# Performance work log

Hardware: AMD Instinct MI355X
Metric: run time of the kernel (lower is better)

Reference implementation:

```python
import jax, jax.numpy as jnp
import numpy as np

FEAT_STRIDE = 16
PRE_NMS = 6000
POST_NMS = 300
NMS_THRESH = 0.7


def _whctrs(a):
    w = a[2] - a[0] + 1.0
    h = a[3] - a[1] + 1.0
    return w, h, a[0] + 0.5 * (w - 1), a[1] + 0.5 * (h - 1)

def _mkanchors(ws, hs, xc, yc):
    return np.stack([xc - 0.5 * (ws - 1), yc - 0.5 * (hs - 1),
                     xc + 0.5 * (ws - 1), yc + 0.5 * (hs - 1)], axis=1)

def _ratio_enum(anchor, ratios):
    w, h, xc, yc = _whctrs(anchor)
    size = w * h
    ws = np.round(np.sqrt(size / ratios))
    hs = np.round(ws * ratios)
    return _mkanchors(ws, hs, xc, yc)

def _scale_enum(anchor, scales):
    w, h, xc, yc = _whctrs(anchor)
    return _mkanchors(w * scales, h * scales, xc, yc)

def generate_anchors(base_size=16, ratios=np.array([0.5, 1.0, 2.0]), scales=np.array([8, 16, 32])):
    base = np.array([1, 1, base_size, base_size], dtype=np.float64) - 1
    ra = _ratio_enum(base, np.asarray(ratios, np.float64))
    return np.vstack([_scale_enum(ra[i], np.asarray(scales, np.float64)) for i in range(ra.shape[0])])


def setup_inputs() -> dict:
    key = jax.random.key(0)
    k1, k2 = jax.random.split(key)
    B, A, H, W = 8, 9, 64, 64
    scores = jax.random.normal(k1, (B, 2 * A, H, W), jnp.float32)
    bbox_deltas = jax.random.normal(k2, (B, 4 * A, H, W), jnp.float32)
    anchors = jnp.asarray(generate_anchors(16), jnp.float32)  # [9, 4]
    return {"scores": scores, "bbox_deltas": bbox_deltas, "anchors": anchors,
            "image_width": 1024, "image_height": 1024}


def _nms_keep(iou, thresh):
    # greedy NMS on score-sorted boxes given a full IoU matrix
    n = iou.shape[0]
    idx = jnp.arange(n)
    def body(i, keep):
        sup = keep[i] & (iou[i] > thresh) & (idx > i)
        return keep & ~sup
    return jax.lax.fori_loop(0, n, body, jnp.ones((n,), bool))


def _nms_one(boxes):  # boxes [PRE_NMS, 4], sorted by score desc
    b = jax.lax.stop_gradient(boxes)
    area = (b[:, 2] - b[:, 0] + 1.0) * (b[:, 3] - b[:, 1] + 1.0)
    iw = jnp.clip(jnp.minimum(b[:, None, 2], b[None, :, 2]) -
                  jnp.maximum(b[:, None, 0], b[None, :, 0]) + 1.0, 0.0)
    ih = jnp.clip(jnp.minimum(b[:, None, 3], b[None, :, 3]) -
                  jnp.maximum(b[:, None, 1], b[None, :, 1]) + 1.0, 0.0)
    inter = iw * ih
    iou = inter / (area[:, None] + area[None, :] - inter)
    keep = _nms_keep(iou, NMS_THRESH)
    # compact kept boxes to the front, pad with zeros (fixed shape)
    rank = jnp.cumsum(keep) - 1
    dest = jnp.where(keep, rank, PRE_NMS)  # suppressed -> dump row
    out = jnp.zeros((PRE_NMS + 1, 4), boxes.dtype).at[dest].set(boxes)
    return out[:POST_NMS]


def _forward(scores, bbox_deltas, anchors, image_width, image_height):
    B = scores.shape[0]
    A = anchors.shape[0]
    H, W = scores.shape[2], scores.shape[3]
    fg = scores[:, A:, :, :]                                   # [B, A, H, W]
    # shifted anchor grid
    mx, my = jnp.meshgrid(jnp.arange(W) * FEAT_STRIDE, jnp.arange(H) * FEAT_STRIDE)
    shifts = jnp.stack([mx.ravel(), my.ravel(), mx.ravel(), my.ravel()], 1).astype(scores.dtype)
    all_anchors = (shifts[:, None, :] + anchors[None, :, :]).reshape(-1, 4)  # [K*A, 4]
    deltas = bbox_deltas.transpose(0, 2, 3, 1).reshape(B, -1, 4)             # [B, K*A, 4]
    sc = fg.transpose(0, 2, 3, 1).reshape(B, -1)                             # [B, K*A]
    # bbox_transform_inv
    aw = all_anchors[:, 2] - all_anchors[:, 0] + 1.0
    ah = all_anchors[:, 3] - all_anchors[:, 1] + 1.0
    acx = all_anchors[:, 0] + 0.5 * aw
    acy = all_anchors[:, 1] + 0.5 * ah
    pcx = deltas[..., 0] * aw + acx
    pcy = deltas[..., 1] * ah + acy
    pw = jnp.exp(deltas[..., 2]) * aw
    ph = jnp.exp(deltas[..., 3]) * ah
    # clip to image
    x1 = jnp.clip(pcx - 0.5 * pw, 0.0, image_width - 1)
    y1 = jnp.clip(pcy - 0.5 * ph, 0.0, image_height - 1)
    x2 = jnp.clip(pcx + 0.5 * pw, 0.0, image_width - 1)
    y2 = jnp.clip(pcy + 0.5 * ph, 0.0, image_height - 1)
    proposals = jnp.stack([x1, y1, x2, y2], -1)                 # [B, K*A, 4]
    # per-image pre-NMS top-k by score
    _, order = jax.lax.top_k(sc, PRE_NMS)
    boxes = jnp.take_along_axis(proposals, order[..., None], axis=1)  # [B, PRE, 4]
    props = jax.lax.map(_nms_one, boxes)                        # [B, POST, 4]
    bidx = jnp.broadcast_to(jnp.arange(B, dtype=props.dtype)[:, None, None], (B, POST_NMS, 1))
    return jnp.concatenate([bidx, props], axis=-1)              # [B, POST, 5]


def reference(scores, bbox_deltas, anchors, image_width, image_height):
    return _forward(scores, bbox_deltas, anchors, image_width, image_height)
```

## Files before the change

### kernel.cpp

```cpp
#include <hip/hip_runtime.h>
#include <math.h>

#pragma clang fp contract(off)

#define BB 8
#define AA 9
#define NPIX 4096
#define NN (NPIX*AA)
#define PRE 6000
#define POST 300
#define SELCAP 7000
#define TMAX 10111
#define HZW 5120

#define RA 0x3F000000u
#define RB 0x41000000u
__device__ __forceinline__ unsigned key_bin2(unsigned k) {
    return (k < RA) ? (k >> 17) : (8064u + ((k - RA) >> 14));
}

#define SMEM_BYTES 65536

__device__ __forceinline__ unsigned score_key(float s) {
    unsigned fb = __float_as_uint(s);
    unsigned u = (fb & 0x80000000u) ? ~fb : (fb | 0x80000000u);
    return ~u;
}

__device__ __forceinline__ unsigned phalf(unsigned v, unsigned bin) {
    return (v >> ((bin & 1) << 4)) & 0xFFFFu;
}

__device__ __forceinline__ bool iou_gt(float ax1, float ay1, float ax2, float ay2, float aa,
                                       float bx1_, float by1_, float bx2_, float by2_, float ab) {
    float xx1 = fmaxf(ax1, bx1_);
    float yy1 = fmaxf(ay1, by1_);
    float xx2 = fminf(ax2, bx2_);
    float yy2 = fminf(ay2, by2_);
    float iw = fmaxf(xx2 - xx1 + 1.0f, 0.0f);
    float ih = fmaxf(yy2 - yy1 + 1.0f, 0.0f);
    float inter = iw * ih;
    float uni = (aa + ab) - inter;
    return (double)inter >= 0x1.666667p-1 * (double)uni;
}

__device__ __forceinline__ void dec_issue(int g, const unsigned short* sorted16,
                                          const float* anch, const float* deltas_b,
                                          float* aw, float* ah, float* acx, float* acy,
                                          float* d0, float* d1, float* d2, float* d3) {
    unsigned idx = sorted16[(g < PRE) ? g : (PRE - 1)];
    int a = (int)(idx % AA);
    int pix = (int)(idx / AA);
    int wq = pix & 63, hq = pix >> 6;
    float sx = (float)(wq * 16), sy = (float)(hq * 16);
    float ax1 = anch[a * 4 + 0] + sx, ay1 = anch[a * 4 + 1] + sy;
    float ax2 = anch[a * 4 + 2] + sx, ay2 = anch[a * 4 + 3] + sy;
    float w_ = ax2 - ax1 + 1.0f, h_ = ay2 - ay1 + 1.0f;
    *aw = w_; *ah = h_;
    *acx = ax1 + 0.5f * w_; *acy = ay1 + 0.5f * h_;
    const float* dp = deltas_b + (size_t)(a * 4) * NPIX + pix;
    *d0 = dp[0]; *d1 = dp[NPIX]; *d2 = dp[2 * NPIX]; *d3 = dp[3 * NPIX];
}

__device__ __forceinline__ void dec_finish(float aw, float ah, float acx, float acy,
                                           float d0, float d1, float d2, float d3,
                                           float fw, float fh, float4* bx, float* ar) {
    float pcx = d0 * aw + acx, pcy = d1 * ah + acy;
    float pw = expf(d2) * aw, ph = expf(d3) * ah;
    float x1 = fminf(fmaxf(pcx - 0.5f * pw, 0.0f), fw);
    float y1 = fminf(fmaxf(pcy - 0.5f * ph, 0.0f), fh);
    float x2 = fminf(fmaxf(pcx + 0.5f * pw, 0.0f), fw);
    float y2 = fminf(fmaxf(pcy + 0.5f * ph, 0.0f), fh);
    *bx = make_float4(x1, y1, x2, y2);
    *ar = (x2 - x1 + 1.0f) * (y2 - y1 + 1.0f);
}

__device__ __forceinline__ void decode_box(int g, const unsigned short* sorted16,
                                           const float* anch, const float* deltas_b,
                                           float fw, float fh, float4* bx, float* ar) {
    float aw, ah, acx, acy, d0, d1, d2, d3;
    dec_issue(g, sorted16, anch, deltas_b, &aw, &ah, &acx, &acy, &d0, &d1, &d2, &d3);
    dec_finish(aw, ah, acx, acy, d0, d1, d2, d3, fw, fh, bx, ar);
}

__device__ __forceinline__ void bar_lds() {
    asm volatile("s_waitcnt lgkmcnt(0)" ::: "memory");
    __builtin_amdgcn_s_barrier();
    asm volatile("" ::: "memory");
}

__global__ __launch_bounds__(1024) void proposal_kernel(const float* __restrict__ scores,
                                                        const float* __restrict__ deltas,
                                                        const float* __restrict__ anchors,
                                                        const int* __restrict__ imw,
                                                        const int* __restrict__ imh,
                                                        float* __restrict__ out) {
    __shared__ __align__(16) unsigned char smem[SMEM_BYTES];
    unsigned*       hist32 = (unsigned*)smem;
    unsigned*       keyh   = (unsigned*)(smem + 20480);
    unsigned short* idxl   = (unsigned short*)(smem + 48512);
    unsigned*       scal   = (unsigned*)(smem + 65344);
    unsigned short* sorted16 = (unsigned short*)(smem + 20480);
    float4*         kb4  = (float4*)smem;
    float*          kba  = (float*)(smem + 4800);
    float4*         cnd4 = (float4*)(smem + 6016);
    float*          cnda = (float*)(smem + 8064);
    unsigned long long* srow  = (unsigned long long*)(smem + 8576);
    unsigned long long* deadw = (unsigned long long*)(smem + 9600);
    float*          anch = (float*)(smem + 9856);

    int b = blockIdx.x;
    int tid = threadIdx.x;
    int wave = tid >> 6, lane = tid & 63;
    const float* sc = scores + (size_t)(b * (2 * AA) + AA) * NPIX;
    const float4* sc4 = (const float4*)sc;
    const float* deltas_b = deltas + (size_t)b * (4 * AA) * NPIX;
    float fw = (float)(imw[0] - 1);
    float fh = (float)(imh[0] - 1);

    for (int j = tid; j < HZW; j += 1024) hist32[j] = 0;
    __syncthreads();
    #pragma unroll
    for (int q = 0; q < 9; ++q) {
        float4 v = sc4[(q << 10) + tid];
        unsigned k0 = score_key(v.x), k1 = score_key(v.y);
        unsigned k2 = score_key(v.z), k3 = score_key(v.w);
        if (k0 < RB) { unsigned b0 = key_bin2(k0); atomicAdd(&hist32[b0 >> 1], 1u << ((b0 & 1) << 4)); }
        if (k1 < RB) { unsigned b1 = key_bin2(k1); atomicAdd(&hist32[b1 >> 1], 1u << ((b1 & 1) << 4)); }
        if (k2 < RB) { unsigned b2 = key_bin2(k2); atomicAdd(&hist32[b2 >> 1], 1u << ((b2 & 1) << 4)); }
        if (k3 < RB) { unsigned b3 = key_bin2(k3); atomicAdd(&hist32[b3 >> 1], 1u << ((b3 & 1) << 4)); }
    }
    __syncthreads();

    unsigned ssum = 0;
    const unsigned* hw = hist32 + tid * 16;
    if (tid < 320) {
        #pragma unroll
        for (int j = 0; j < 16; ++j) { unsigned w = hw[j]; ssum += (w & 0xFFFFu) + (w >> 16); }
    }
    unsigned x = ssum;
    #pragma unroll
    for (int d = 1; d < 64; d <<= 1) {
        unsigned y = __shfl_up(x, (unsigned)d, 64);
        if (lane >= d) x += y;
    }
    if (lane == 63 && wave < 5) scal[wave] = x;
    __syncthreads();
    unsigned wexcl = 0;
    #pragma unroll
    for (int w = 0; w < 5; ++w) if (w < wave) wexcl += scal[w];
    unsigned gexcl = wexcl + (x - ssum);
    unsigned gincl = gexcl + ssum;
    if (tid == 319) { scal[16] = TMAX; scal[17] = gincl; }
    __syncthreads();
    if (tid < 320 && gexcl <= (PRE - 1) && (PRE - 1) < gincl) {
        unsigned c = gexcl, T = tid * 32, tot = gincl;
        bool f = false;
        for (int j = 0; j < 32 && !f; ++j) {
            unsigned d = phalf(hw[j >> 1], (unsigned)j);
            if ((PRE - 1) < c + d) { T = tid * 32 + j; tot = c + d; f = true; }
            c += d;
        }
        scal[16] = T;
        scal[17] = tot;
    }
    __syncthreads();
    unsigned T = scal[16];
    if (T > TMAX) T = TMAX;
    unsigned cnt = scal[17];
    if (cnt > SELCAP) cnt = SELCAP;

    if ((unsigned)(tid * 32) <= T) {
        unsigned run = gexcl;
        unsigned* wv = hist32 + tid * 16;
        #pragma unroll
        for (int j = 0; j < 16; ++j) {
            unsigned v = wv[j];
            unsigned c0 = v & 0xFFFFu, c1 = v >> 16;
            wv[j] = run | ((run + c0) << 16);
            run += c0 + c1;
        }
    }
    __syncthreads();

    #pragma unroll
    for (int q = 0; q < 9; ++q) {
        float4 v = sc4[(q << 10) + tid];
        #pragma unroll
        for (int c = 0; c < 4; ++c) {
            float s = (c == 0) ? v.x : (c == 1) ? v.y : (c == 2) ? v.z : v.w;
            unsigned k = score_key(s);
            if (k < RB) {
                unsigned bin = key_bin2(k);
                if (bin <= T) {
                    unsigned old = atomicAdd(&hist32[bin >> 1], 1u << ((bin & 1) << 4));
                    unsigned pos = phalf(old, bin);
                    if (pos < SELCAP) {
                        keyh[pos] = k;
                        int pix = (tid << 2) + c;
                        idxl[pos] = (unsigned short)(pix * AA + q);
                    }
                }
            }
        }
    }
    __syncthreads();

    unsigned rnk8[8], id8[8];
    #pragma unroll
    for (int m = 0; m < 8; ++m) {
        int s = (m << 10) + tid;
        rnk8[m] = 0xFFFFFFFFu;
        if (s < (int)cnt) {
            unsigned k = keyh[s];
            unsigned id = idxl[s];
            unsigned bin = key_bin2(k);
            unsigned start = bin ? phalf(hist32[(bin - 1) >> 1], bin - 1) : 0u;
            unsigned end = phalf(hist32[bin >> 1], bin);
            if (end > cnt) end = cnt;
            if (start > end) start = end;
            unsigned rank = start;
            for (unsigned j = start; j < end; ++j) {
                unsigned kj = keyh[j];
                rank += (kj < k) ? 1u : 0u;
                if (kj == k) rank += ((unsigned)idxl[j] < id) ? 1u : 0u;
            }
            rnk8[m] = rank;
            id8[m] = id;
        }
    }
    __syncthreads();
    #pragma unroll
    for (int m = 0; m < 8; ++m)
        if (rnk8[m] < PRE) sorted16[rnk8[m]] = (unsigned short)id8[m];
    if (tid < 36) anch[tid] = anchors[tid];
    __syncthreads();

    float s_aw = 0.f, s_ah = 0.f, s_acx = 0.f, s_acy = 0.f;
    float s_d0 = 0.f, s_d1 = 0.f, s_d2 = 0.f, s_d3 = 0.f;

    if (tid < 64) {
        float4 bx; float ar;
        decode_box(tid, sorted16, anch, deltas_b, fw, fh, &bx, &ar);
        cnd4[tid] = bx; cnda[tid] = ar;
    }
    if (wave == 8)
        dec_issue(64 + lane, sorted16, anch, deltas_b,
                  &s_aw, &s_ah, &s_acx, &s_acy, &s_d0, &s_d1, &s_d2, &s_d3);
    __syncthreads();

    int cur = 0, K = 0, p = 0, pb = 0;
    for (;;) {
        float4 mc = cnd4[p * 64 + lane];
        float ma = cnda[p * 64 + lane];

        if (wave == 8) {
            float4 nb; float na;
            dec_finish(s_aw, s_ah, s_acx, s_acy, s_d0, s_d1, s_d2, s_d3,
                       fw, fh, &nb, &na);
            cnd4[(p ^ 1) * 64 + lane] = nb;
            cnda[(p ^ 1) * 64 + lane] = na;
            dec_issue(cur + 128 + lane, sorted16, anch, deltas_b,
                      &s_aw, &s_ah, &s_acx, &s_acy, &s_d0, &s_d1, &s_d2, &s_d3);
        }

        bool dead = (cur + lane >= PRE);
        if (wave != 8) {
            int w15 = (wave < 8) ? wave : (wave - 1);
            for (int k = w15; k < K; k += 15) {
                float4 kv = kb4[k];
                float ka = kba[k];
                dead = dead || iou_gt(kv.x, kv.y, kv.z, kv.w, ka, mc.x, mc.y, mc.z, mc.w, ma);
            }
        }
        unsigned long long db = __ballot(dead);
        if (lane == 0) deadw[pb * 16 + wave] = db;

        #pragma unroll
        for (int q2 = 0; q2 < 4; ++q2) {
            int j = (q2 << 4) + wave;
            float4 cj = cnd4[p * 64 + j];
            float aj = cnda[p * 64 + j];
            bool g = (lane < j) && iou_gt(mc.x, mc.y, mc.z, mc.w, ma,
                                          cj.x, cj.y, cj.z, cj.w, aj);
            unsigned long long bl = __ballot(g);
            if (lane == 0) srow[pb * 64 + j] = bl;
        }

        bar_lds();

        unsigned long long dk = deadw[pb * 16 + 0];
        #pragma unroll
        for (int w = 1; w < 16; ++w) dk |= deadw[pb * 16 + w];
        unsigned long long row = srow[pb * 64 + lane];
        unsigned long long live = ~dk;
        unsigned long long keptb = 0ULL;
        int allowed = POST - K;
        while (live) {
            int f = __ffsll((long long)live) - 1;
            keptb |= (1ULL << f);
            if (__popcll(keptb) >= allowed) break;
            bool die = (row >> f) & 1ULL;
            unsigned long long dbl = __ballot(die);
            live &= ~(dbl | (1ULL << f));
        }
        int nkeep = __popcll(keptb);
        int take = (nkeep < allowed) ? nkeep : allowed;

        if ((keptb >> lane) & 1ULL) {
            int rnk = __popcll(keptb & ((1ULL << lane) - 1ULL));
            if (rnk < take) { kb4[K + rnk] = mc; kba[K + rnk] = ma; }
        }
        K += take;
        cur += 64;
        if (K >= POST || cur >= PRE) break;
        p ^= 1; pb ^= 1;
    }

    __syncthreads();
    for (int idx = tid; idx < POST * 5; idx += 1024) {
        int row_ = idx / 5;
        int col = idx - row_ * 5;
        float val = 0.0f;
        if (row_ < K) {
            float4 v = kb4[row_];
            val = (col == 0) ? (float)b : (col == 1) ? v.x : (col == 2) ? v.y
                : (col == 3) ? v.z : v.w;
        }
        out[(size_t)b * POST * 5 + idx] = val;
    }
}

extern "C" void kernel_launch(void* const* d_in, const int* in_sizes, int n_in,
                              void* d_out, int out_size, void* d_ws, size_t ws_size,
                              hipStream_t stream) {
    const float* scores  = (const float*)d_in[0];
    const float* deltas  = (const float*)d_in[1];
    const float* anchors = (const float*)d_in[2];
    const int*   imw     = (const int*)d_in[3];
    const int*   imh     = (const int*)d_in[4];
    float* out = (float*)d_out;

    proposal_kernel<<<BB, 1024, 0, stream>>>(scores, deltas, anchors, imw, imh, out);
}
```

Before: 145.7 us.

## Parallelize kept-box suppression check over lanes per candidate with early exit

The check of each 64-candidate chunk against already-kept boxes is reorganized. Before, each wave looped serially over kept boxes with one candidate per lane. Now each wave owns 4-5 candidates and tests all kept boxes in parallel across lanes, stopping early once a candidate is found dead. Per-candidate dead flags are stored as bytes and combined with a ballot. The intent is to shorten the serial loop over K, which can reach 300 kept boxes, at the cost of more ballots and less even work across waves.

```diff
diff --git a/kernel.cpp b/kernel.cpp
--- a/kernel.cpp
+++ b/kernel.cpp
@@ -106,7 +106,7 @@
     float4*         cnd4 = (float4*)(smem + 6016);
     float*          cnda = (float*)(smem + 8064);
     unsigned long long* srow  = (unsigned long long*)(smem + 8576);
-    unsigned long long* deadw = (unsigned long long*)(smem + 9600);
+    unsigned char*  dead8 = (unsigned char*)(smem + 9600);
     float*          anch = (float*)(smem + 9856);
 
     int b = blockIdx.x;
@@ -253,6 +253,14 @@
     for (;;) {
         float4 mc = cnd4[p * 64 + lane];
         float ma = cnda[p * 64 + lane];
+        float4 cj0 = cnd4[p * 64 + wave];
+        float4 cj1 = cnd4[p * 64 + 16 + wave];
+        float4 cj2 = cnd4[p * 64 + 32 + wave];
+        float4 cj3 = cnd4[p * 64 + 48 + wave];
+        float aj0 = cnda[p * 64 + wave];
+        float aj1 = cnda[p * 64 + 16 + wave];
+        float aj2 = cnda[p * 64 + 32 + wave];
+        float aj3 = cnda[p * 64 + 48 + wave];
 
         if (wave == 8) {
             float4 nb; float na;
@@ -264,34 +272,63 @@
                       &s_aw, &s_ah, &s_acx, &s_acy, &s_d0, &s_d1, &s_d2, &s_d3);
         }
 
-        bool dead = (cur + lane >= PRE);
         if (wave != 8) {
             int w15 = (wave < 8) ? wave : (wave - 1);
-            for (int k = w15; k < K; k += 15) {
-                float4 kv = kb4[k];
-                float ka = kba[k];
-                dead = dead || iou_gt(kv.x, kv.y, kv.z, kv.w, ka, mc.x, mc.y, mc.z, mc.w, ma);
+            int nc = (w15 < 4) ? 5 : 4;
+            int cstart = (w15 < 4) ? (w15 * 5) : (20 + (w15 - 4) * 4);
+            for (int ci = 0; ci < nc; ++ci) {
+                int cand = cstart + ci;
+                float4 cb = cnd4[p * 64 + cand];
+                float cba = cnda[p * 64 + cand];
+                bool deadc = (cur + cand >= PRE);
+                for (int t = 0; (t << 6) < K && !deadc; ++t) {
+                    int k = (t << 6) + lane;
+                    bool hit = false;
+                    if (k < K) {
+                        float4 kv = kb4[k];
+                        float ka = kba[k];
+                        hit = iou_gt(kv.x, kv.y, kv.z, kv.w, ka,
+                                     cb.x, cb.y, cb.z, cb.w, cba);
+                    }
+                    deadc = (__ballot(hit) != 0ULL);
+                }
+                if (lane == 0) dead8[pb * 64 + cand] = deadc ? 1 : 0;
             }
         }
-        unsigned long long db = __ballot(dead);
-        if (lane == 0) deadw[pb * 16 + wave] = db;
-
-        #pragma unroll
-        for (int q2 = 0; q2 < 4; ++q2) {
-            int j = (q2 << 4) + wave;
-            float4 cj = cnd4[p * 64 + j];
-            float aj = cnda[p * 64 + j];
+
+        {
+            int j = wave;
             bool g = (lane < j) && iou_gt(mc.x, mc.y, mc.z, mc.w, ma,
-                                          cj.x, cj.y, cj.z, cj.w, aj);
+                                          cj0.x, cj0.y, cj0.z, cj0.w, aj0);
             unsigned long long bl = __ballot(g);
             if (lane == 0) srow[pb * 64 + j] = bl;
         }
+        {
+            int j = 16 + wave;
+            bool g = (lane < j) && iou_gt(mc.x, mc.y, mc.z, mc.w, ma,
+                                          cj1.x, cj1.y, cj1.z, cj1.w, aj1);
+            unsigned long long bl = __ballot(g);
+            if (lane == 0) srow[pb * 64 + j] = bl;
+        }
+        {
+            int j = 32 + wave;
+            bool g = (lane < j) && iou_gt(mc.x, mc.y, mc.z, mc.w, ma,
+                                          cj2.x, cj2.y, cj2.z, cj2.w, aj2);
+            unsigned long long bl = __ballot(g);
+            if (lane == 0) srow[pb * 64 + j] = bl;
+        }
+        {
+            int j = 48 + wave;
+            bool g = (lane < j) && iou_gt(mc.x, mc.y, mc.z, mc.w, ma,
+                                          cj3.x, cj3.y, cj3.z, cj3.w, aj3);
+            unsigned long long bl = __ballot(g);
+            if (lane == 0) srow[pb * 64 + j] = bl;
+        }
 
         bar_lds();
 
-        unsigned long long dk = deadw[pb * 16 + 0];
-        #pragma unroll
-        for (int w = 1; w < 16; ++w) dk |= deadw[pb * 16 + w];
+        bool dead = dead8[pb * 64 + lane] != 0;
+        unsigned long long dk = __ballot(dead);
         unsigned long long row = srow[pb * 64 + lane];
         unsigned long long live = ~dk;
         unsigned long long keptb = 0ULL;
```

Result: no change. 148.2 us (+1.7%).

## Parallelize NMS kept-box checks across lanes and compute IoU rows only for survivors

Applied to the files above, without the earlier changes.

The 15 non-decoder waves no longer each walk a strided slice of kept boxes per candidate lane. Each wave now owns 4-5 candidates and tests all kept boxes across its 64 lanes, then reduces with a ballot into a per-candidate dead byte. The intra-chunk suppression matrix is then built only for surviving candidates, indexed by rank, which cuts IoU work when many candidates are already dead. In exchange it adds a second barrier phase with serial rank-to-index bit scans. The dead-flag computation moves to the LDS-synchronised step before the matrix build, so the double-buffered pb state is removed.

```diff
diff --git a/kernel.cpp b/kernel.cpp
--- a/kernel.cpp
+++ b/kernel.cpp
@@ -105,9 +105,9 @@
     float*          kba  = (float*)(smem + 4800);
     float4*         cnd4 = (float4*)(smem + 6016);
     float*          cnda = (float*)(smem + 8064);
-    unsigned long long* srow  = (unsigned long long*)(smem + 8576);
-    unsigned long long* deadw = (unsigned long long*)(smem + 9600);
-    float*          anch = (float*)(smem + 9856);
+    unsigned long long* srow_s = (unsigned long long*)(smem + 8576);
+    unsigned char*  dead8 = (unsigned char*)(smem + 9088);
+    float*          anch = (float*)(smem + 9216);
 
     int b = blockIdx.x;
     int tid = threadIdx.x;
@@ -249,7 +249,11 @@
                   &s_aw, &s_ah, &s_acx, &s_acy, &s_d0, &s_d1, &s_d2, &s_d3);
     __syncthreads();
 
-    int cur = 0, K = 0, p = 0, pb = 0;
+    int w15 = (wave < 8) ? wave : (wave - 1);
+    int nc = (w15 < 4) ? 5 : 4;
+    int cstart = (w15 < 4) ? (w15 * 5) : (20 + (w15 - 4) * 4);
+
+    int cur = 0, K = 0, p = 0;
     for (;;) {
         float4 mc = cnd4[p * 64 + lane];
         float ma = cnda[p * 64 + lane];
@@ -262,38 +266,61 @@
             cnda[(p ^ 1) * 64 + lane] = na;
             dec_issue(cur + 128 + lane, sorted16, anch, deltas_b,
                       &s_aw, &s_ah, &s_acx, &s_acy, &s_d0, &s_d1, &s_d2, &s_d3);
-        }
-
-        bool dead = (cur + lane >= PRE);
-        if (wave != 8) {
-            int w15 = (wave < 8) ? wave : (wave - 1);
-            for (int k = w15; k < K; k += 15) {
-                float4 kv = kb4[k];
-                float ka = kba[k];
-                dead = dead || iou_gt(kv.x, kv.y, kv.z, kv.w, ka, mc.x, mc.y, mc.z, mc.w, ma);
+        } else {
+            int kk = (K < 64) ? K : 64;
+            bool kval = (lane < kk);
+            int kidx = kval ? lane : 0;
+            float4 kv = kb4[kidx];
+            float  ka = kba[kidx];
+            #pragma unroll
+            for (int ci = 0; ci < 5; ++ci) {
+                if (ci >= nc) break;
+                int cand = cstart + ci;
+                float4 cb = cnd4[p * 64 + cand];
+                float cba = cnda[p * 64 + cand];
+                bool dd = (cur + cand >= PRE);
+                bool hit = kval && iou_gt(kv.x, kv.y, kv.z, kv.w, ka,
+                                          cb.x, cb.y, cb.z, cb.w, cba);
+                if (__ballot(hit) != 0ULL) dd = true;
+                if (!dd && K > 64) {
+                    bool any = false;
+                    for (int base = 64; base < K; base += 64) {
+                        int kj = base + lane;
+                        bool v2 = (kj < K);
+                        int kc = v2 ? kj : 0;
+                        float4 kv2 = kb4[kc];
+                        float  ka2 = kba[kc];
+                        any = any | (v2 && iou_gt(kv2.x, kv2.y, kv2.z, kv2.w, ka2,
+                                                  cb.x, cb.y, cb.z, cb.w, cba));
+                    }
+                    if (__ballot(any) != 0ULL) dd = true;
+                }
+                if (lane == 0) dead8[cand] = dd ? 1 : 0;
             }
         }
-        unsigned long long db = __ballot(dead);
-        if (lane == 0) deadw[pb * 16 + wave] = db;
-
-        #pragma unroll
-        for (int q2 = 0; q2 < 4; ++q2) {
-            int j = (q2 << 4) + wave;
+
+        bar_lds();
+
+        bool slive = (dead8[lane] == 0);
+        unsigned long long surv = __ballot(slive);
+        int nsurv = __popcll(surv);
+        for (int rk = wave; rk < nsurv; rk += 16) {
+            unsigned long long m = surv;
+            for (int i = 0; i < rk; ++i) m &= (m - 1);
+            int j = __ffsll((long long)m) - 1;
             float4 cj = cnd4[p * 64 + j];
-            float aj = cnda[p * 64 + j];
+            float  aj = cnda[p * 64 + j];
             bool g = (lane < j) && iou_gt(mc.x, mc.y, mc.z, mc.w, ma,
                                           cj.x, cj.y, cj.z, cj.w, aj);
             unsigned long long bl = __ballot(g);
-            if (lane == 0) srow[pb * 64 + j] = bl;
+            if (lane == 0) srow_s[rk] = bl;
         }
 
         bar_lds();
 
-        unsigned long long dk = deadw[pb * 16 + 0];
-        #pragma unroll
-        for (int w = 1; w < 16; ++w) dk |= deadw[pb * 16 + w];
-        unsigned long long row = srow[pb * 64 + lane];
-        unsigned long long live = ~dk;
+        int myrk = __popcll(surv & ((1ULL << lane) - 1ULL));
+        unsigned long long row = slive ? srow_s[myrk] : 0ULL;
+        unsigned long long live = surv;
         unsigned long long keptb = 0ULL;
         int allowed = POST - K;
         while (live) {
@@ -314,7 +341,7 @@
         K += take;
         cur += 64;
         if (K >= POST || cur >= PRE) break;
-        p ^= 1; pb ^= 1;
+        p ^= 1;
     }
 
     __syncthreads();
```

Result: slower. 181.5 us (+24.6%).
